# Kernel tuning notes

Hardware: AMD Instinct MI355X
Metric: run time of the kernel (lower is better)

## Reference

```python
import jax, jax.numpy as jnp
import numpy as np

N_HEADS = 16


def setup_inputs() -> dict:
    key = jax.random.key(0)
    ks = jax.random.split(key, 9)
    B, S, D = 4, 2048, 1024
    query = jax.random.normal(ks[0], (B, S, D), dtype=jnp.float32)
    key_t = jax.random.normal(ks[1], (B, S, D), dtype=jnp.float32)
    value = jax.random.normal(ks[2], (B, S, D), dtype=jnp.float32)
    mask = jax.random.randint(ks[3], (B, 1, S, S), 0, 10) > 0
    scale_w = 0.02  # keep exp(attention) in a safe range
    Wq = jax.random.normal(ks[4], (D, D), dtype=jnp.float32) * scale_w
    Wk = jax.random.normal(ks[5], (D, D), dtype=jnp.float32) * scale_w
    Wv = jax.random.normal(ks[6], (D, D), dtype=jnp.float32) * scale_w
    fc_w = jax.random.normal(ks[7], (D, D), dtype=jnp.float32) * scale_w
    fc_b = jnp.zeros((D,), dtype=jnp.float32)
    return {"query": query, "key": key_t, "value": value, "mask": mask,
            "Wq": Wq, "Wk": Wk, "Wv": Wv, "fc_w": fc_w, "fc_b": fc_b}


def reference(query, key, value, mask, Wq, Wk, Wv, fc_w, fc_b):
    B, S, D = query.shape
    H = N_HEADS
    Dh = D // H
    scale = jnp.sqrt(jnp.asarray(D / H, dtype=query.dtype))
    # Faithful to original: direct reshape [B,S,D] -> [B,H,S,Dh] (no transpose)
    Q = (query @ Wq.T).reshape(B, H, S, Dh)
    K = (key @ Wk.T).reshape(B, H, S, Dh)
    V = (value @ Wv.T).reshape(B, H, S, Dh)
    attn = jnp.einsum('bhqd,bhkd->bhqk', Q, K) / scale  # [B,H,S,S]
    # Hand-rolled masked softmax: exp, masked_fill(False->0), normalize, nan->0
    temp = jnp.where(mask, jnp.exp(attn), 0.0)
    attn = temp / jnp.sum(temp, axis=-1, keepdims=True)
    attn = jnp.where(jnp.isnan(attn), 0.0, attn)
    res = jnp.einsum('bhqk,bhkd->bhqd', attn, V)  # [B,H,S,Dh]
    outs = res.transpose(0, 2, 1, 3).reshape(B, S, D)
    outs = outs @ fc_w.T + fc_b
    return outs, res.transpose(1, 0, 2, 3)
```

## Files before the change

### kernel.cpp

```cpp
#include <hip/hip_runtime.h>


typedef __attribute__((ext_vector_type(8))) short bf16x8;
typedef __attribute__((ext_vector_type(4))) short bf16x4;
typedef __attribute__((ext_vector_type(4))) float f32x4;

#define MFMA32(a, b, c) __builtin_amdgcn_mfma_f32_16x16x32_bf16(a, b, c, 0, 0, 0)

#if __has_builtin(__builtin_amdgcn_mfma_f32_16x16x16bf16_1k)
#define MFMA_K16(a, b, c) __builtin_amdgcn_mfma_f32_16x16x16bf16_1k(a, b, c, 0, 0, 0)
#else
static __device__ __forceinline__ f32x4 mfma_k16_asm(bf16x4 a, bf16x4 b, f32x4 c) {
  f32x4 d;
  asm volatile("v_mfma_f32_16x16x16_bf16 %0, %1, %2, %3\n\ts_nop 7\n\ts_nop 7"
               : "=v"(d) : "v"(a), "v"(b), "v"(c));
  return d;
}
#define MFMA_K16(a, b, c) mfma_k16_asm(a, b, c)
#endif

static __device__ __forceinline__ float fast_exp2(float x) {
#if __has_builtin(__builtin_amdgcn_exp2f)
  return __builtin_amdgcn_exp2f(x);
#else
  return __expf(x * 0.69314718056f);
#endif
}

__device__ __forceinline__ unsigned short fbf(float f) {
  union { float f; unsigned u; } x; x.f = f;
  unsigned r = x.u + 0x7fffu + ((x.u >> 16) & 1u);
  return (unsigned short)(r >> 16);
}

static __device__ __forceinline__ bf16x4 pack2(unsigned lo, unsigned hi) {
  union { unsigned u[2]; bf16x4 v; } x; x.u[0] = lo; x.u[1] = hi; return x.v;
}

static __device__ __forceinline__ bf16x4 epp(f32x4 s, unsigned pre, int sh) {
  union { float f; unsigned u; } e0, e1, e2, e3;
  e0.f = fast_exp2(s[0]); e1.f = fast_exp2(s[1]);
  e2.f = fast_exp2(s[2]); e3.f = fast_exp2(s[3]);
  unsigned p01 = __builtin_amdgcn_perm(e1.u + 0x8000u, e0.u + 0x8000u, 0x07060302u);
  unsigned p23 = __builtin_amdgcn_perm(e3.u + 0x8000u, e2.u + 0x8000u, 0x07060302u);
  int m0 = __builtin_amdgcn_sbfe(pre, sh + 0, 1), m1 = __builtin_amdgcn_sbfe(pre, sh + 1, 1);
  int m2 = __builtin_amdgcn_sbfe(pre, sh + 2, 1), m3 = __builtin_amdgcn_sbfe(pre, sh + 3, 1);
  unsigned k01 = __builtin_amdgcn_perm((unsigned)m1, (unsigned)m0, 0x07060100u);
  unsigned k23 = __builtin_amdgcn_perm((unsigned)m3, (unsigned)m2, 0x07060100u);
  return pack2(p01 & k01, p23 & k23);
}

__global__ __launch_bounds__(256) void f2b3_kernel(const float* __restrict__ s0,
                                                   const float* __restrict__ s1,
                                                   const float* __restrict__ s2,
                                                   unsigned short* __restrict__ d0,
                                                   unsigned short* __restrict__ d1,
                                                   unsigned short* __restrict__ d2) {
  int z = blockIdx.y;
  const float* s = (z == 0) ? s0 : (z == 1) ? s1 : s2;
  unsigned short* d = (z == 0) ? d0 : (z == 1) ? d1 : d2;
  int i = blockIdx.x * 256 + threadIdx.x;
  float4 v = ((const float4*)s)[i];
  ushort4 o;
  o.x = fbf(v.x); o.y = fbf(v.y); o.z = fbf(v.z); o.w = fbf(v.w);
  ((ushort4*)d)[i] = o;
}

__global__ __launch_bounds__(256) void f2b4_kernel(const float* __restrict__ s0,
                                                   const float* __restrict__ s1,
                                                   const float* __restrict__ s2,
                                                   const float* __restrict__ s3,
                                                   unsigned short* __restrict__ d0,
                                                   unsigned short* __restrict__ d1,
                                                   unsigned short* __restrict__ d2,
                                                   unsigned short* __restrict__ d3) {
  int z = blockIdx.y;
  const float* s = (z == 0) ? s0 : (z == 1) ? s1 : (z == 2) ? s2 : s3;
  unsigned short* d = (z == 0) ? d0 : (z == 1) ? d1 : (z == 2) ? d2 : d3;
  int i = blockIdx.x * 256 + threadIdx.x;
  float4 v = ((const float4*)s)[i];
  ushort4 o;
  o.x = fbf(v.x); o.y = fbf(v.y); o.z = fbf(v.z); o.w = fbf(v.w);
  ((ushort4*)d)[i] = o;
}

__global__ __launch_bounds__(256) void pack_mask_kernel(const int* __restrict__ m,
                                                        unsigned long long* __restrict__ o) {
  int i = blockIdx.x * 256 + threadIdx.x;
  unsigned long long b = __ballot(m[i] != 0);
  if ((threadIdx.x & 63) == 0) o[i >> 6] = b;
}

__global__ __launch_bounds__(256) void proj_kernel(const unsigned short* __restrict__ A0,
                                                   const unsigned short* __restrict__ A1,
                                                   const unsigned short* __restrict__ A2,
                                                   const unsigned short* __restrict__ W0,
                                                   const unsigned short* __restrict__ W1,
                                                   const unsigned short* __restrict__ W2,
                                                   unsigned short* __restrict__ C0,
                                                   unsigned short* __restrict__ C1,
                                                   unsigned short* __restrict__ C2) {
  __shared__ unsigned short Alds[128 * 32];
  __shared__ unsigned short Blds[128 * 32];
  const int z = blockIdx.z;
  const unsigned short* A = (z == 0) ? A0 : (z == 1) ? A1 : A2;
  const unsigned short* B = (z == 0) ? W0 : (z == 1) ? W1 : W2;
  const int tid = threadIdx.x;
  const int w = tid >> 6, l = tid & 63, q4 = l >> 4, c16 = l & 15;
  const int wm = w & 1, wn = w >> 1;
  const int mBase = blockIdx.y * 128, nBase = blockIdx.x * 128;

  f32x4 acc[4][4];
#pragma unroll
  for (int a0 = 0; a0 < 4; ++a0)
#pragma unroll
    for (int a1 = 0; a1 < 4; ++a1) acc[a0][a1] = (f32x4){0.f, 0.f, 0.f, 0.f};

  const int r0 = tid >> 2, cc0 = tid & 3;

  for (int kt = 0; kt < 32; ++kt) {
    __syncthreads();
    const unsigned short* ga0 = A + (mBase + r0) * 1024 + kt * 32 + cc0 * 8;
    const unsigned short* ga1 = A + (mBase + 64 + r0) * 1024 + kt * 32 + cc0 * 8;
    const unsigned short* gb0 = B + (nBase + r0) * 1024 + kt * 32 + cc0 * 8;
    const unsigned short* gb1 = B + (nBase + 64 + r0) * 1024 + kt * 32 + cc0 * 8;
    __builtin_amdgcn_global_load_lds((const __attribute__((address_space(1))) void*)ga0,
                                     (__attribute__((address_space(3))) void*)(&Alds[tid * 8]),
                                     16, 0, 0);
    __builtin_amdgcn_global_load_lds((const __attribute__((address_space(1))) void*)ga1,
                                     (__attribute__((address_space(3))) void*)(&Alds[(tid + 256) * 8]),
                                     16, 0, 0);
    __builtin_amdgcn_global_load_lds((const __attribute__((address_space(1))) void*)gb0,
                                     (__attribute__((address_space(3))) void*)(&Blds[tid * 8]),
                                     16, 0, 0);
    __builtin_amdgcn_global_load_lds((const __attribute__((address_space(1))) void*)gb1,
                                     (__attribute__((address_space(3))) void*)(&Blds[(tid + 256) * 8]),
                                     16, 0, 0);
    __syncthreads();

    bf16x8 af[4], bfr[4];
#pragma unroll
    for (int mi = 0; mi < 4; ++mi)
      af[mi] = *(const bf16x8*)&Alds[(wm * 64 + mi * 16 + c16) * 32 + q4 * 8];
#pragma unroll
    for (int ni = 0; ni < 4; ++ni)
      bfr[ni] = *(const bf16x8*)&Blds[(wn * 64 + ni * 16 + c16) * 32 + q4 * 8];
#pragma unroll
    for (int mi = 0; mi < 4; ++mi)
#pragma unroll
      for (int ni = 0; ni < 4; ++ni) acc[mi][ni] = MFMA32(af[mi], bfr[ni], acc[mi][ni]);
  }

  const float scale = (z == 0) ? 0.18033688f : 1.0f;
#pragma unroll
  for (int mi = 0; mi < 4; ++mi) {
#pragma unroll
    for (int ni = 0; ni < 4; ++ni) {
#pragma unroll
      for (int rg = 0; rg < 4; ++rg) {
        int row = mBase + wm * 64 + mi * 16 + q4 * 4 + rg;
        int col = nBase + wn * 64 + ni * 16 + c16;
        float v = acc[mi][ni][rg];
        if (z < 2) {
          unsigned short* C = (z == 0) ? C0 : C1;
          C[row * 1024 + col] = fbf(v * scale);
        } else {
          int bb = row >> 11, rr = row & 2047;
          int hh = rr >> 7;
          int ss = ((rr & 127) << 4) | (col >> 6);
          int dh = col & 63;
          C2[((bb * 16 + hh) * 64 + dh) * 2048 + ss] = fbf(v);
        }
      }
    }
  }
}

__global__ __launch_bounds__(256) void gemm_out(const unsigned short* __restrict__ A,
                                                const unsigned short* __restrict__ B,
                                                float* __restrict__ C,
                                                const float* __restrict__ bias) {
  __shared__ unsigned short Alds[128 * 32];
  __shared__ unsigned short Blds[128 * 32];
  const int tid = threadIdx.x;
  const int w = tid >> 6, l = tid & 63, q4 = l >> 4, c16 = l & 15;
  const int wm = w & 1, wn = w >> 1;
  const int mBase = blockIdx.y * 128, nBase = blockIdx.x * 128;

  f32x4 acc[4][4];
#pragma unroll
  for (int a0 = 0; a0 < 4; ++a0)
#pragma unroll
    for (int a1 = 0; a1 < 4; ++a1) acc[a0][a1] = (f32x4){0.f, 0.f, 0.f, 0.f};

  const int r0 = tid >> 2, cc0 = tid & 3;

  for (int kt = 0; kt < 32; ++kt) {
    __syncthreads();
    const unsigned short* ga0 = A + (mBase + r0) * 1024 + kt * 32 + cc0 * 8;
    const unsigned short* ga1 = A + (mBase + 64 + r0) * 1024 + kt * 32 + cc0 * 8;
    const unsigned short* gb0 = B + (nBase + r0) * 1024 + kt * 32 + cc0 * 8;
    const unsigned short* gb1 = B + (nBase + 64 + r0) * 1024 + kt * 32 + cc0 * 8;
    __builtin_amdgcn_global_load_lds((const __attribute__((address_space(1))) void*)ga0,
                                     (__attribute__((address_space(3))) void*)(&Alds[tid * 8]),
                                     16, 0, 0);
    __builtin_amdgcn_global_load_lds((const __attribute__((address_space(1))) void*)ga1,
                                     (__attribute__((address_space(3))) void*)(&Alds[(tid + 256) * 8]),
                                     16, 0, 0);
    __builtin_amdgcn_global_load_lds((const __attribute__((address_space(1))) void*)gb0,
                                     (__attribute__((address_space(3))) void*)(&Blds[tid * 8]),
                                     16, 0, 0);
    __builtin_amdgcn_global_load_lds((const __attribute__((address_space(1))) void*)gb1,
                                     (__attribute__((address_space(3))) void*)(&Blds[(tid + 256) * 8]),
                                     16, 0, 0);
    __syncthreads();

    bf16x8 af[4], bfr[4];
#pragma unroll
    for (int mi = 0; mi < 4; ++mi)
      af[mi] = *(const bf16x8*)&Alds[(wm * 64 + mi * 16 + c16) * 32 + q4 * 8];
#pragma unroll
    for (int ni = 0; ni < 4; ++ni)
      bfr[ni] = *(const bf16x8*)&Blds[(wn * 64 + ni * 16 + c16) * 32 + q4 * 8];
#pragma unroll
    for (int mi = 0; mi < 4; ++mi)
#pragma unroll
      for (int ni = 0; ni < 4; ++ni) acc[mi][ni] = MFMA32(af[mi], bfr[ni], acc[mi][ni]);
  }

#pragma unroll
  for (int mi = 0; mi < 4; ++mi) {
#pragma unroll
    for (int ni = 0; ni < 4; ++ni) {
#pragma unroll
      for (int rg = 0; rg < 4; ++rg) {
        int row = mBase + wm * 64 + mi * 16 + q4 * 4 + rg;
        int col = nBase + wn * 64 + ni * 16 + c16;
        C[row * 1024 + col] = acc[mi][ni][rg] + bias[col];
      }
    }
  }
}

__global__ __launch_bounds__(256) void flash_kernel(const unsigned short* __restrict__ Q,
                                                    const unsigned short* __restrict__ K,
                                                    const unsigned short* __restrict__ Vt,
                                                    const uint4* __restrict__ mb,
                                                    unsigned short* __restrict__ Cws,
                                                    float* __restrict__ res2) {
  __shared__ unsigned short Klds[128 * 64];
  __shared__ unsigned short Vtlds[64 * 128];
  const int tid = threadIdx.x;
  const int w = tid >> 6, l = tid & 63, q4 = l >> 4, c16 = l & 15;
  const int q44 = q4 * 4;
  const int qt = blockIdx.x, h = blockIdx.y, b = blockIdx.z;
  const unsigned short* Qh = Q + (b * 2048 + h * 128) * 1024;
  const unsigned short* Kh = K + (b * 2048 + h * 128) * 1024;
  const unsigned short* Vth = Vt + (b * 16 + h) * 64 * 2048;

  bf16x8 qf[2][2];
#pragma unroll
  for (int i = 0; i < 2; ++i)
#pragma unroll
    for (int kc = 0; kc < 2; ++kc)
      qf[i][kc] = *(const bf16x8*)(Qh + (qt * 128 + w * 32 + i * 16 + c16) * 64 + kc * 32 + q4 * 8);

  const uint4* mrow0 = mb + (b * 2048 + qt * 128 + w * 32 + c16) * 16;
  const uint4* mrow1 = mrow0 + 16 * 16;

  const int kOff = (tid >> 3) * 64 + (((tid & 7) ^ ((tid >> 3) & 7)) * 8);
  const int vOff = (tid >> 4) * 2048 + (((tid & 15) ^ (tid >> 4)) * 8);

  const int kb0 = c16 * 64 + ((q4 ^ (c16 & 7)) * 8);
  const int kb1 = kb0 ^ 32;
  const int vbase = c16 * 128 + (q4 & 1) * 4;
  const int c16e = c16 & 14;
  const int lowb = (q4 >> 1) ^ (c16 & 1);

  const bf16x4 kOnes = {(short)0x3F80, (short)0x3F80, (short)0x3F80, (short)0x3F80};

  f32x4 oacc[2][4], soacc[2];
#pragma unroll
  for (int i = 0; i < 2; ++i) {
    soacc[i] = (f32x4){0.f, 0.f, 0.f, 0.f};
#pragma unroll
    for (int t = 0; t < 4; ++t) oacc[i][t] = (f32x4){0.f, 0.f, 0.f, 0.f};
  }

  for (int kt = 0; kt < 16; ++kt) {
    const unsigned short* gk = Kh + kt * 8192 + kOff;
    const unsigned short* gv = Vth + kt * 128 + vOff;
#pragma unroll
    for (int j = 0; j < 4; ++j) {
      __builtin_amdgcn_global_load_lds((const __attribute__((address_space(1))) void*)(gk + j * 2048),
                                       (__attribute__((address_space(3))) void*)(&Klds[(j * 256 + tid) * 8]),
                                       16, 0, 0);
      __builtin_amdgcn_global_load_lds((const __attribute__((address_space(1))) void*)(gv + j * 32768),
                                       (__attribute__((address_space(3))) void*)(&Vtlds[(j * 256 + tid) * 8]),
                                       16, 0, 0);
    }
    uint4 m0 = mrow0[kt], m1 = mrow1[kt];
    unsigned pre0[4] = {m0.x >> q44, m0.y >> q44, m0.z >> q44, m0.w >> q44};
    unsigned pre1[4] = {m1.x >> q44, m1.y >> q44, m1.z >> q44, m1.w >> q44};
    __syncthreads();

#pragma unroll
    for (int n = 0; n < 8; ++n) {
      bf16x8 kf0 = *(const bf16x8*)(Klds + kb0 + n * 1024);
      bf16x8 kf1 = *(const bf16x8*)(Klds + kb1 + n * 1024);
      f32x4 s0 = (f32x4){0.f, 0.f, 0.f, 0.f}, s1 = (f32x4){0.f, 0.f, 0.f, 0.f};
      s0 = MFMA32(kf0, qf[0][0], s0);
      s0 = MFMA32(kf1, qf[0][1], s0);
      s1 = MFMA32(kf0, qf[1][0], s1);
      s1 = MFMA32(kf1, qf[1][1], s1);

      int sh = (n & 1) * 16;
      bf16x4 pp0 = epp(s0, pre0[n >> 1], sh);
      bf16x4 pp1 = epp(s1, pre1[n >> 1], sh);

      int gsn = ((2 * n) ^ c16e) | lowb;
      int va = vbase + gsn * 8;
#pragma unroll
      for (int t = 0; t < 4; ++t) {
        bf16x4 vf = *(const bf16x4*)(Vtlds + va + t * 2048);
        oacc[0][t] = MFMA_K16(vf, pp0, oacc[0][t]);
        oacc[1][t] = MFMA_K16(vf, pp1, oacc[1][t]);
      }
      soacc[0] = MFMA_K16(kOnes, pp0, soacc[0]);
      soacc[1] = MFMA_K16(kOnes, pp1, soacc[1]);
    }
    __syncthreads();
  }

#pragma unroll
  for (int i = 0; i < 2; ++i) {
    float sum = soacc[i][0];
    float rcp = (sum > 0.f) ? (1.0f / sum) : 0.f;
    int q = qt * 128 + w * 32 + i * 16 + c16;
    float* rp = res2 + (((h * 4 + b) * 2048 + q) * 64 + q44);
    unsigned short* cp = Cws + ((b * 2048 + q) * 1024 + h * 64 + q44);
#pragma unroll
    for (int t = 0; t < 4; ++t) {
      float o0 = oacc[i][t][0] * rcp, o1 = oacc[i][t][1] * rcp;
      float o2 = oacc[i][t][2] * rcp, o3 = oacc[i][t][3] * rcp;
      float4 fo = {o0, o1, o2, o3};
      *(float4*)(rp + t * 16) = fo;
      ushort4 cv = {fbf(o0), fbf(o1), fbf(o2), fbf(o3)};
      *(ushort4*)(cp + t * 16) = cv;
    }
  }
}

extern "C" void kernel_launch(void* const* d_in, const int* in_sizes, int n_in,
                              void* d_out, int out_size, void* d_ws, size_t ws_size,
                              hipStream_t stream) {
  const float* query = (const float*)d_in[0];
  const float* key_t = (const float*)d_in[1];
  const float* value = (const float*)d_in[2];
  const int* mask = (const int*)d_in[3];
  const float* Wq = (const float*)d_in[4];
  const float* Wk = (const float*)d_in[5];
  const float* Wv = (const float*)d_in[6];
  const float* fcw = (const float*)d_in[7];
  const float* fcb = (const float*)d_in[8];
  float* out = (float*)d_out;

  char* ws = (char*)d_ws;
  unsigned short* qbf = (unsigned short*)(ws);
  unsigned short* kbf = (unsigned short*)(ws + (16u << 20));
  unsigned short* vbf = (unsigned short*)(ws + (32u << 20));
  unsigned short* wqb = (unsigned short*)(ws + (48u << 20));
  unsigned short* wkb = (unsigned short*)(ws + (50u << 20));
  unsigned short* wvb = (unsigned short*)(ws + (52u << 20));
  unsigned short* fwb = (unsigned short*)(ws + (54u << 20));
  unsigned short* Qf = (unsigned short*)(ws + (56u << 20));
  unsigned short* Kf = (unsigned short*)(ws + (72u << 20));
  unsigned short* Vt = (unsigned short*)(ws + (88u << 20));
  unsigned short* Cws = qbf;
  unsigned long long* mbits = (unsigned long long*)kbf;

  f2b3_kernel<<<dim3(8192, 3), 256, 0, stream>>>(query, key_t, value, qbf, kbf, vbf);
  f2b4_kernel<<<dim3(1024, 4), 256, 0, stream>>>(Wq, Wk, Wv, fcw, wqb, wkb, wvb, fwb);

  proj_kernel<<<dim3(8, 64, 3), 256, 0, stream>>>(qbf, kbf, vbf, wqb, wkb, wvb, Qf, Kf, Vt);

  pack_mask_kernel<<<65536, 256, 0, stream>>>(mask, mbits);

  flash_kernel<<<dim3(16, 16, 4), 256, 0, stream>>>(Qf, Kf, Vt, (const uint4*)mbits, Cws,
                                                    out + 8388608);

  gemm_out<<<dim3(8, 64), 256, 0, stream>>>(Cws, fwb, out, fcb);
}
```

Before: 483.9 us.

## Use K=32 MFMA for PV by pairing score tiles; retile mask layout

The flash kernel now computes two adjacent 16-key score tiles per step and concatenates their exponentiated bf16 probabilities into an 8-wide fragment. This lets the PV and row-sum products use the 16x16x32 MFMA instead of twice as many 16x16x16 MFMAs. The packed mask is stored in a kt-major layout so per-tile mask loads from adjacent rows are contiguous. A launch_bounds occupancy hint of 4 blocks is added, which raises register pressure because more scores are live at once.

```diff
diff --git a/kernel.cpp b/kernel.cpp
--- a/kernel.cpp
+++ b/kernel.cpp
@@ -6,18 +6,6 @@
 typedef __attribute__((ext_vector_type(4))) float f32x4;
 
 #define MFMA32(a, b, c) __builtin_amdgcn_mfma_f32_16x16x32_bf16(a, b, c, 0, 0, 0)
-
-#if __has_builtin(__builtin_amdgcn_mfma_f32_16x16x16bf16_1k)
-#define MFMA_K16(a, b, c) __builtin_amdgcn_mfma_f32_16x16x16bf16_1k(a, b, c, 0, 0, 0)
-#else
-static __device__ __forceinline__ f32x4 mfma_k16_asm(bf16x4 a, bf16x4 b, f32x4 c) {
-  f32x4 d;
-  asm volatile("v_mfma_f32_16x16x16_bf16 %0, %1, %2, %3\n\ts_nop 7\n\ts_nop 7"
-               : "=v"(d) : "v"(a), "v"(b), "v"(c));
-  return d;
-}
-#define MFMA_K16(a, b, c) mfma_k16_asm(a, b, c)
-#endif
 
 static __device__ __forceinline__ float fast_exp2(float x) {
 #if __has_builtin(__builtin_amdgcn_exp2f)
@@ -35,6 +23,10 @@
 
 static __device__ __forceinline__ bf16x4 pack2(unsigned lo, unsigned hi) {
   union { unsigned u[2]; bf16x4 v; } x; x.u[0] = lo; x.u[1] = hi; return x.v;
+}
+
+static __device__ __forceinline__ bf16x8 cat2(bf16x4 lo, bf16x4 hi) {
+  union { bf16x4 h[2]; bf16x8 v; } x; x.h[0] = lo; x.h[1] = hi; return x.v;
 }
 
 static __device__ __forceinline__ bf16x4 epp(f32x4 s, unsigned pre, int sh) {
@@ -88,7 +80,12 @@
                                                         unsigned long long* __restrict__ o) {
   int i = blockIdx.x * 256 + threadIdx.x;
   unsigned long long b = __ballot(m[i] != 0);
-  if ((threadIdx.x & 63) == 0) o[i >> 6] = b;
+  if ((threadIdx.x & 63) == 0) {
+    int row = i >> 11;
+    int kt = (i >> 7) & 15;
+    int h = (i >> 6) & 1;
+    o[(kt * 8192 + row) * 2 + h] = b;
+  }
 }
 
 __global__ __launch_bounds__(256) void proj_kernel(const unsigned short* __restrict__ A0,
@@ -242,12 +239,12 @@
   }
 }
 
-__global__ __launch_bounds__(256) void flash_kernel(const unsigned short* __restrict__ Q,
-                                                    const unsigned short* __restrict__ K,
-                                                    const unsigned short* __restrict__ Vt,
-                                                    const uint4* __restrict__ mb,
-                                                    unsigned short* __restrict__ Cws,
-                                                    float* __restrict__ res2) {
+__global__ __launch_bounds__(256, 4) void flash_kernel(const unsigned short* __restrict__ Q,
+                                                       const unsigned short* __restrict__ K,
+                                                       const unsigned short* __restrict__ Vt,
+                                                       const uint4* __restrict__ mb,
+                                                       unsigned short* __restrict__ Cws,
+                                                       float* __restrict__ res2) {
   __shared__ unsigned short Klds[128 * 64];
   __shared__ unsigned short Vtlds[64 * 128];
   const int tid = threadIdx.x;
@@ -265,19 +262,18 @@
     for (int kc = 0; kc < 2; ++kc)
       qf[i][kc] = *(const bf16x8*)(Qh + (qt * 128 + w * 32 + i * 16 + c16) * 64 + kc * 32 + q4 * 8);
 
-  const uint4* mrow0 = mb + (b * 2048 + qt * 128 + w * 32 + c16) * 16;
-  const uint4* mrow1 = mrow0 + 16 * 16;
+  const int rowi = b * 2048 + qt * 128 + w * 32 + c16;
 
   const int kOff = (tid >> 3) * 64 + (((tid & 7) ^ ((tid >> 3) & 7)) * 8);
   const int vOff = (tid >> 4) * 2048 + (((tid & 15) ^ (tid >> 4)) * 8);
 
   const int kb0 = c16 * 64 + ((q4 ^ (c16 & 7)) * 8);
   const int kb1 = kb0 ^ 32;
-  const int vbase = c16 * 128 + (q4 & 1) * 4;
-  const int c16e = c16 & 14;
-  const int lowb = (q4 >> 1) ^ (c16 & 1);
-
-  const bf16x4 kOnes = {(short)0x3F80, (short)0x3F80, (short)0x3F80, (short)0x3F80};
+  const int vb = c16 * 128 + (q4 & 1) * 4;
+  const int q41 = q4 >> 1;
+
+  const bf16x8 ones8 = {(short)0x3F80, (short)0x3F80, (short)0x3F80, (short)0x3F80,
+                        (short)0x3F80, (short)0x3F80, (short)0x3F80, (short)0x3F80};
 
   f32x4 oacc[2][4], soacc[2];
 #pragma unroll
@@ -299,35 +295,41 @@
                                        (__attribute__((address_space(3))) void*)(&Vtlds[(j * 256 + tid) * 8]),
                                        16, 0, 0);
     }
-    uint4 m0 = mrow0[kt], m1 = mrow1[kt];
+    uint4 m0 = mb[kt * 8192 + rowi];
+    uint4 m1 = mb[kt * 8192 + rowi + 16];
     unsigned pre0[4] = {m0.x >> q44, m0.y >> q44, m0.z >> q44, m0.w >> q44};
     unsigned pre1[4] = {m1.x >> q44, m1.y >> q44, m1.z >> q44, m1.w >> q44};
     __syncthreads();
 
 #pragma unroll
-    for (int n = 0; n < 8; ++n) {
-      bf16x8 kf0 = *(const bf16x8*)(Klds + kb0 + n * 1024);
-      bf16x8 kf1 = *(const bf16x8*)(Klds + kb1 + n * 1024);
-      f32x4 s0 = (f32x4){0.f, 0.f, 0.f, 0.f}, s1 = (f32x4){0.f, 0.f, 0.f, 0.f};
-      s0 = MFMA32(kf0, qf[0][0], s0);
-      s0 = MFMA32(kf1, qf[0][1], s0);
-      s1 = MFMA32(kf0, qf[1][0], s1);
-      s1 = MFMA32(kf1, qf[1][1], s1);
-
-      int sh = (n & 1) * 16;
-      bf16x4 pp0 = epp(s0, pre0[n >> 1], sh);
-      bf16x4 pp1 = epp(s1, pre1[n >> 1], sh);
-
-      int gsn = ((2 * n) ^ c16e) | lowb;
-      int va = vbase + gsn * 8;
+    for (int m = 0; m < 4; ++m) {
+      bf16x8 kfE0 = *(const bf16x8*)(Klds + kb0 + (2 * m) * 1024);
+      bf16x8 kfE1 = *(const bf16x8*)(Klds + kb1 + (2 * m) * 1024);
+      bf16x8 kfO0 = *(const bf16x8*)(Klds + kb0 + (2 * m + 1) * 1024);
+      bf16x8 kfO1 = *(const bf16x8*)(Klds + kb1 + (2 * m + 1) * 1024);
+      f32x4 sE0 = {0.f, 0.f, 0.f, 0.f}, sE1 = {0.f, 0.f, 0.f, 0.f};
+      f32x4 sO0 = {0.f, 0.f, 0.f, 0.f}, sO1 = {0.f, 0.f, 0.f, 0.f};
+      sE0 = MFMA32(kfE0, qf[0][0], sE0); sE0 = MFMA32(kfE1, qf[0][1], sE0);
+      sE1 = MFMA32(kfE0, qf[1][0], sE1); sE1 = MFMA32(kfE1, qf[1][1], sE1);
+      sO0 = MFMA32(kfO0, qf[0][0], sO0); sO0 = MFMA32(kfO1, qf[0][1], sO0);
+      sO1 = MFMA32(kfO0, qf[1][0], sO1); sO1 = MFMA32(kfO1, qf[1][1], sO1);
+
+      int shE = 0, shO = 16;
+      bf16x8 pf0 = cat2(epp(sE0, pre0[m], shE), epp(sO0, pre0[m], shO));
+      bf16x8 pf1 = cat2(epp(sE1, pre1[m], shE), epp(sO1, pre1[m], shO));
+
+      int pLo = (4 * m + q41) ^ c16;
+      int aLo = vb + pLo * 8;
 #pragma unroll
       for (int t = 0; t < 4; ++t) {
-        bf16x4 vf = *(const bf16x4*)(Vtlds + va + t * 2048);
-        oacc[0][t] = MFMA_K16(vf, pp0, oacc[0][t]);
-        oacc[1][t] = MFMA_K16(vf, pp1, oacc[1][t]);
+        bf16x4 vlo = *(const bf16x4*)(Vtlds + aLo + t * 2048);
+        bf16x4 vhi = *(const bf16x4*)(Vtlds + (aLo ^ 16) + t * 2048);
+        bf16x8 vf8 = cat2(vlo, vhi);
+        oacc[0][t] = MFMA32(vf8, pf0, oacc[0][t]);
+        oacc[1][t] = MFMA32(vf8, pf1, oacc[1][t]);
       }
-      soacc[0] = MFMA_K16(kOnes, pp0, soacc[0]);
-      soacc[1] = MFMA_K16(kOnes, pp1, soacc[1]);
+      soacc[0] = MFMA32(ones8, pf0, soacc[0]);
+      soacc[1] = MFMA32(ones8, pf1, soacc[1]);
     }
     __syncthreads();
   }
```

Result: faster. 460.6 us (-4.8%).
